# Kernel tuning notes

Measured on AMD Instinct MI355X. Metric: run time of the kernel, lower is better.

## Reference

```python
import jax, jax.numpy as jnp
import numpy as np

B, N, F_IN, F_OUT, T, K = 2, 4096, 16, 16, 12, 3


def setup_inputs() -> dict:
    key = jax.random.key(0)
    k1, k2, k3, k4 = jax.random.split(key, 4)
    x = jax.random.normal(k1, (B, N, F_IN, T), dtype=jnp.float32)
    # stacked K Chebyshev polynomial matrices T_k(L~), each (N, N)
    cheb_polynomials = jax.random.normal(k2, (K, N, N), dtype=jnp.float32) / np.sqrt(N)
    # ChebNetII interpolation table: cheb_poly_xj[j, k] = T_k evaluated at node x_j (scalar)
    cheb_poly_xj = jax.random.normal(k3, (K, K), dtype=jnp.float32)
    # learned Gamma_j parameters, each (F_in, F_out)
    Gamma = jax.random.normal(k4, (K, F_IN, F_OUT), dtype=jnp.float32) * 0.1
    return {"x": x, "cheb_polynomials": cheb_polynomials,
            "cheb_poly_xj": cheb_poly_xj, "Gamma": Gamma}


def reference(x, cheb_polynomials, cheb_poly_xj, Gamma):
    # x: (B, N, F_in, T); cheb_polynomials: (K, N, N);
    # cheb_poly_xj: (K, K) scalars; Gamma: (K, F_in, F_out)
    K_ = Gamma.shape[0]
    # lhs_k = sum_j Gamma_j * cheb_poly_xj[j, k]  -> (K, F_in, F_out); hoisted out of T loop
    lhs = jnp.einsum('jio,jk->kio', Gamma, cheb_poly_xj)
    # project features first (small contraction): (K, B, N, F_out, T)
    z = jnp.einsum('bmft,kfo->kbmot', x, lhs)
    # graph propagation: rhs[b,n,f] = sum_m x[b,m,f] * T_k[m, n]  (note T_k applied on the right)
    out = jnp.einsum('kmn,kbmot->bnot', cheb_polynomials, z)
    return jax.nn.relu((2.0 / (K_ + 1)) * out)
```

## Files before the change

kernel.cpp:

```cpp
#include <hip/hip_runtime.h>
#include <stdint.h>

typedef float    f32x4 __attribute__((ext_vector_type(4)));
typedef _Float16 f16x8 __attribute__((ext_vector_type(8)));
typedef unsigned int u32x4 __attribute__((ext_vector_type(4)));

#define NN     4096
#define KTOT   12288
#define CDIM   384
#define BN     128
#define BK     32
#define TSTEPS 384

__global__ __launch_bounds__(256) void zbuild_kernel(
    const float* __restrict__ x,
    const float* __restrict__ xj,
    const float* __restrict__ gamma,
    _Float16* __restrict__ zws)
{
  __shared__ float xs[32 * 193];
  __shared__ float lhs[768];
  const int tid = threadIdx.x;
  const int b   = blockIdx.x & 1;
  const int m0  = (blockIdx.x >> 1) << 5;

  for (int e = tid; e < 768; e += 256) {
    const int k = e >> 8, fo = e & 255;
    float s = 0.f;
#pragma unroll
    for (int j = 0; j < 3; ++j) s += gamma[j * 256 + fo] * xj[j * 3 + k];
    lhs[e] = s;
  }
  const float* xsrc = x + (size_t)(b * 4096 + m0) * 192;
  for (int q = tid; q < 1536; q += 256) {
    const int fl  = q << 2;
    const int ml  = fl / 192;
    const int off = fl - ml * 192;
    const f32x4 v = *(const f32x4*)(xsrc + fl);
#pragma unroll
    for (int r = 0; r < 4; ++r) xs[ml * 193 + off + r] = v[r];
  }
  __syncthreads();

  for (int slot = tid; slot < 512; slot += 256) {
    const int ml = slot & 31, o = slot >> 5;
    float acc[3][12];
#pragma unroll
    for (int k = 0; k < 3; ++k)
#pragma unroll
      for (int t = 0; t < 12; ++t) acc[k][t] = 0.f;

#pragma unroll
    for (int f = 0; f < 16; ++f) {
      float xv[12];
#pragma unroll
      for (int t = 0; t < 12; ++t) xv[t] = xs[ml * 193 + f * 12 + t];
#pragma unroll
      for (int k = 0; k < 3; ++k) {
        const float lf = lhs[k * 256 + f * 16 + o];
#pragma unroll
        for (int t = 0; t < 12; ++t) acc[k][t] += xv[t] * lf;
      }
    }
    const int mg = m0 + ml;
    const int cb = b * 192 + o * 12;
#pragma unroll
    for (int k = 0; k < 3; ++k)
#pragma unroll
      for (int t = 0; t < 12; ++t)
        zws[(size_t)(cb + t) * KTOT + k * 4096 + mg] = (_Float16)acc[k][t];
  }
}

__global__ __launch_bounds__(512, 2) void gemm_kernel(
    const float* __restrict__ cheb,
    const _Float16* __restrict__ zws,
    float* __restrict__ partials,
    int S, int spb)
{
  __shared__ unsigned short As[2][CDIM * BK];
  __shared__ unsigned short Bs[2][BN * BK];

  const int tid  = threadIdx.x;
  const int by   = blockIdx.x % S;
  const int bx   = blockIdx.x / S;
  const int lane = tid & 63, wid = tid >> 6;
  const int l15  = lane & 15, l4 = lane >> 4;
  const int wc   = wid >> 1, wn = wid & 1;
  const int nbase = bx * BN;
  const int step0 = by * spb;
  int nsteps = TSTEPS - step0;
  if (nsteps > spb) nsteps = spb;
  if (nsteps < 0) nsteps = 0;

  f32x4 acc[6][4];
#pragma unroll
  for (int mi = 0; mi < 6; ++mi)
#pragma unroll
    for (int ni = 0; ni < 4; ++ni) acc[mi][ni] = (f32x4)(0.f);

  const int ia0 = wid * 192 + lane;
  const int rrB = tid >> 5;
  const int n4B = (tid & 31) << 2;

  u32x4 areg[3];
  f32x4 breg[2];

  auto LOADA = [&](int t) {
    const size_t mb = (size_t)(step0 + t) * (BK * 2);
#pragma unroll
    for (int j = 0; j < 3; ++j) {
      const int i = ia0 + j * 64;
      const char* p = (const char*)zws + (size_t)(i >> 2) * (KTOT * 2) + mb + (i & 3) * 16;
      areg[j] = *(const u32x4*)p;
    }
  };
  auto LOADB = [&](int t) {
    const int m0g = (step0 + t) * BK;
#pragma unroll
    for (int s = 0; s < 2; ++s) {
      const int m = rrB * 2 + s;
      breg[s] = *(const f32x4*)(cheb + (size_t)(m0g + m) * NN + nbase + n4B);
    }
  };
  auto WRITEA = [&](int buf) {
#pragma unroll
    for (int j = 0; j < 3; ++j) {
      const int i   = ia0 + j * 64;
      const int c   = i >> 2;
      const int blk = i ^ ((c >> 1) & 3);
      *(u32x4*)&As[buf][blk * 8] = areg[j];
    }
  };
  auto WRITEB = [&](int buf) {
#pragma unroll
    for (int d = 0; d < 4; ++d) {
      const _Float16 h0 = (_Float16)breg[0][d];
      const _Float16 h1 = (_Float16)breg[1][d];
      const int n   = n4B + d;
      const int us0 = n * BK + rrB * 2;
      int blk = us0 >> 3;
      blk ^= (n >> 2) & 7;
      const int usp = blk * 8 + (us0 & 7);
      const uint32_t w = (uint32_t)__builtin_bit_cast(unsigned short, h0) |
                         ((uint32_t)__builtin_bit_cast(unsigned short, h1) << 16);
      *(uint32_t*)&Bs[buf][usp] = w;
    }
  };
  auto COMPUTE = [&](int cur) {
    f16x8 af[6];
#pragma unroll
    for (int mi = 0; mi < 6; ++mi) {
      const int c   = wc * 96 + mi * 16 + l15;
      const int i   = c * 4 + l4;
      const int blk = i ^ ((c >> 1) & 3);
      af[mi] = *(const f16x8*)&As[cur][blk * 8];
    }
    f16x8 bf[4];
#pragma unroll
    for (int ni = 0; ni < 4; ++ni) {
      const int n   = wn * 64 + ni * 16 + l15;
      const int blk = (n * 4 + l4) ^ ((n >> 2) & 7);
      bf[ni] = *(const f16x8*)&Bs[cur][blk * 8];
    }
#pragma unroll
    for (int mi = 0; mi < 6; ++mi)
#pragma unroll
      for (int ni = 0; ni < 4; ++ni)
        acc[mi][ni] = __builtin_amdgcn_mfma_f32_16x16x32_f16(
            af[mi], bf[ni], acc[mi][ni], 0, 0, 0);
  };

  if (nsteps > 0) {
    LOADA(0); LOADB(0);
    WRITEA(0); WRITEB(0);
    __syncthreads();
    for (int t = 0; t < nsteps; ++t) {
      const int cur = t & 1;
      const bool pf = (t + 1 < nsteps);
      if (pf) { LOADA(t + 1); LOADB(t + 1); }
      COMPUTE(cur);
      if (pf) { WRITEA(cur ^ 1); WRITEB(cur ^ 1); }
      __syncthreads();
    }
  }

  float* pb = partials + (size_t)by * ((size_t)CDIM * NN);
#pragma unroll
  for (int mi = 0; mi < 6; ++mi) {
    const int c0 = wc * 96 + mi * 16 + l4 * 4;
#pragma unroll
    for (int ni = 0; ni < 4; ++ni) {
      const int n = nbase + wn * 64 + ni * 16 + l15;
#pragma unroll
      for (int r = 0; r < 4; ++r)
        pb[(size_t)(c0 + r) * NN + n] = acc[mi][ni][r];
    }
  }
}

__global__ __launch_bounds__(256) void reduce_kernel(
    const float* __restrict__ partials, float* __restrict__ out, int S)
{
  __shared__ float T[192 * 33];
  const int tid = threadIdx.x;
  const int n0  = blockIdx.x * 32;
  const int cb  = blockIdx.y;

  for (int i = tid; i < 6144; i += 256) {
    const int c_l = i >> 5, n_l = i & 31;
    const float* p = partials + (size_t)(cb * 192 + c_l) * NN + n0 + n_l;
    float s = 0.f;
    for (int ss = 0; ss < S; ++ss) s += p[(size_t)ss * ((size_t)CDIM * NN)];
    T[c_l * 33 + n_l] = s;
  }
  __syncthreads();
  for (int j = tid; j < 6144; j += 256) {
    const int n_l = j / 192, ot = j - n_l * 192;
    const float v = 0.5f * T[ot * 33 + n_l];
    out[(size_t)(cb * 4096 + n0 + n_l) * 192 + ot] = v > 0.f ? v : 0.f;
  }
}

extern "C" void kernel_launch(void* const* d_in, const int* in_sizes, int n_in,
                              void* d_out, int out_size, void* d_ws, size_t ws_size,
                              hipStream_t stream) {
  (void)in_sizes; (void)n_in; (void)out_size;
  const float* x     = (const float*)d_in[0];
  const float* cheb  = (const float*)d_in[1];
  const float* xj    = (const float*)d_in[2];
  const float* gamma = (const float*)d_in[3];
  float* out = (float*)d_out;

  const long long zbytes = (long long)CDIM * KTOT * 2;
  const long long pslab  = (long long)CDIM * NN * 4;
  int S = 8;
  const long long avail = (long long)ws_size - zbytes;
  if (avail < 8 * pslab) {
    S = (int)(avail / pslab);
    if (S < 1) S = 1;
    if (S > 8) S = 8;
  }
  const int spb = (TSTEPS + S - 1) / S;

  _Float16* zws   = (_Float16*)d_ws;
  float* partials = (float*)((char*)d_ws + zbytes);

  zbuild_kernel<<<256, 256, 0, stream>>>(x, xj, gamma, zws);
  gemm_kernel<<<32 * S, 512, 0, stream>>>(cheb, zws, partials, S, spb);
  reduce_kernel<<<dim3(128, 2), 256, 0, stream>>>(partials, out, S);
}
```

Baseline: 365.5 us.

## Load GEMM A fragments directly to registers, halve N tile, raise occupancy

The GEMM no longer stages the z operand (A) in shared memory. Each wave loads its MFMA A fragments straight from global memory into registers, double-buffered across steps. The N tile drops from 128 to 64, doubling the block count, and launch bounds now allow 4 blocks per CU since shared memory only holds B. This removes LDS traffic and bank conflicts for A, at the cost of more global/L2 reads of A (each block re-reads it for a smaller N slice) and less B reuse per block.

```diff
diff --git a/kernel.cpp b/kernel.cpp
--- a/kernel.cpp
+++ b/kernel.cpp
@@ -1,6 +1,7 @@
 #include <hip/hip_runtime.h>
 #include <stdint.h>
 
+typedef float    f32x2 __attribute__((ext_vector_type(2)));
 typedef float    f32x4 __attribute__((ext_vector_type(4)));
 typedef _Float16 f16x8 __attribute__((ext_vector_type(8)));
 typedef unsigned int u32x4 __attribute__((ext_vector_type(4)));
@@ -8,7 +9,7 @@
 #define NN     4096
 #define KTOT   12288
 #define CDIM   384
-#define BN     128
+#define BN     64
 #define BK     32
 #define TSTEPS 384
 
@@ -72,126 +73,102 @@
   }
 }
 
-__global__ __launch_bounds__(512, 2) void gemm_kernel(
+__global__ __launch_bounds__(512, 4) void gemm_kernel(
     const float* __restrict__ cheb,
     const _Float16* __restrict__ zws,
     float* __restrict__ partials,
     int S, int spb)
 {
-  __shared__ unsigned short As[2][CDIM * BK];
-  __shared__ unsigned short Bs[2][BN * BK];
+  __shared__ unsigned int Bs[2][BN * BK / 2];
 
   const int tid  = threadIdx.x;
   const int by   = blockIdx.x % S;
   const int bx   = blockIdx.x / S;
   const int lane = tid & 63, wid = tid >> 6;
   const int l15  = lane & 15, l4 = lane >> 4;
-  const int wc   = wid >> 1, wn = wid & 1;
   const int nbase = bx * BN;
   const int step0 = by * spb;
   int nsteps = TSTEPS - step0;
   if (nsteps > spb) nsteps = spb;
   if (nsteps < 0) nsteps = 0;
 
-  f32x4 acc[6][4];
-#pragma unroll
-  for (int mi = 0; mi < 6; ++mi)
+  f32x4 acc[3][4];
+#pragma unroll
+  for (int mi = 0; mi < 3; ++mi)
 #pragma unroll
     for (int ni = 0; ni < 4; ++ni) acc[mi][ni] = (f32x4)(0.f);
 
-  const int ia0 = wid * 192 + lane;
-  const int rrB = tid >> 5;
-  const int n4B = (tid & 31) << 2;
-
-  u32x4 areg[3];
-  f32x4 breg[2];
-
-  auto LOADA = [&](int t) {
-    const size_t mb = (size_t)(step0 + t) * (BK * 2);
-#pragma unroll
-    for (int j = 0; j < 3; ++j) {
-      const int i = ia0 + j * 64;
-      const char* p = (const char*)zws + (size_t)(i >> 2) * (KTOT * 2) + mb + (i & 3) * 16;
-      areg[j] = *(const u32x4*)p;
-    }
-  };
+  const int rr = tid >> 5;
+  const int nn = (tid & 31) << 1;
+  f32x2 b0, b1;
   auto LOADB = [&](int t) {
-    const int m0g = (step0 + t) * BK;
-#pragma unroll
-    for (int s = 0; s < 2; ++s) {
-      const int m = rrB * 2 + s;
-      breg[s] = *(const f32x4*)(cheb + (size_t)(m0g + m) * NN + nbase + n4B);
-    }
-  };
-  auto WRITEA = [&](int buf) {
-#pragma unroll
-    for (int j = 0; j < 3; ++j) {
-      const int i   = ia0 + j * 64;
-      const int c   = i >> 2;
-      const int blk = i ^ ((c >> 1) & 3);
-      *(u32x4*)&As[buf][blk * 8] = areg[j];
-    }
+    const float* base = cheb + (size_t)(step0 + t) * BK * NN + nbase + nn;
+    b0 = *(const f32x2*)(base + (size_t)(2 * rr)     * NN);
+    b1 = *(const f32x2*)(base + (size_t)(2 * rr + 1) * NN);
   };
   auto WRITEB = [&](int buf) {
 #pragma unroll
-    for (int d = 0; d < 4; ++d) {
-      const _Float16 h0 = (_Float16)breg[0][d];
-      const _Float16 h1 = (_Float16)breg[1][d];
-      const int n   = n4B + d;
-      const int us0 = n * BK + rrB * 2;
-      int blk = us0 >> 3;
-      blk ^= (n >> 2) & 7;
-      const int usp = blk * 8 + (us0 & 7);
+    for (int d = 0; d < 2; ++d) {
+      const int n = nn + d;
+      const _Float16 h0 = (_Float16)b0[d], h1 = (_Float16)b1[d];
       const uint32_t w = (uint32_t)__builtin_bit_cast(unsigned short, h0) |
                          ((uint32_t)__builtin_bit_cast(unsigned short, h1) << 16);
-      *(uint32_t*)&Bs[buf][usp] = w;
-    }
-  };
-  auto COMPUTE = [&](int cur) {
-    f16x8 af[6];
-#pragma unroll
-    for (int mi = 0; mi < 6; ++mi) {
-      const int c   = wc * 96 + mi * 16 + l15;
-      const int i   = c * 4 + l4;
-      const int blk = i ^ ((c >> 1) & 3);
-      af[mi] = *(const f16x8*)&As[cur][blk * 8];
-    }
+      const int blk = (n * 4 + (rr >> 2)) ^ ((n >> 2) & 3);
+      Bs[buf][blk * 4 + (rr & 3)] = w;
+    }
+  };
+
+  const char* abase = (const char*)zws +
+      (size_t)(wid * 48 + l15) * (KTOT * 2) + (size_t)l4 * 16;
+  auto LOADA = [&](int t, u32x4* ar) {
+    const size_t kb = (size_t)(step0 + t) * (BK * 2);
+#pragma unroll
+    for (int mi = 0; mi < 3; ++mi)
+      ar[mi] = *(const u32x4*)(abase + (size_t)mi * 16 * (KTOT * 2) + kb);
+  };
+
+  auto STEP = [&](int t, u32x4* arCur, u32x4* arNxt, int cur) {
+    const bool pf = (t + 1 < nsteps);
+    if (pf) LOADB(t + 1);
     f16x8 bf[4];
 #pragma unroll
     for (int ni = 0; ni < 4; ++ni) {
-      const int n   = wn * 64 + ni * 16 + l15;
-      const int blk = (n * 4 + l4) ^ ((n >> 2) & 7);
-      bf[ni] = *(const f16x8*)&Bs[cur][blk * 8];
-    }
-#pragma unroll
-    for (int mi = 0; mi < 6; ++mi)
+      const int n   = ni * 16 + l15;
+      const int blk = (n * 4 + l4) ^ ((n >> 2) & 3);
+      bf[ni] = *(const f16x8*)&Bs[cur][blk * 4];
+    }
+    if (pf) LOADA(t + 1, arNxt);
+#pragma unroll
+    for (int mi = 0; mi < 3; ++mi) {
+      const f16x8 af = __builtin_bit_cast(f16x8, arCur[mi]);
 #pragma unroll
       for (int ni = 0; ni < 4; ++ni)
         acc[mi][ni] = __builtin_amdgcn_mfma_f32_16x16x32_f16(
-            af[mi], bf[ni], acc[mi][ni], 0, 0, 0);
-  };
-
+            af, bf[ni], acc[mi][ni], 0, 0, 0);
+    }
+    if (pf) WRITEB(cur ^ 1);
+    __syncthreads();
+  };
+
+  u32x4 arA[3], arB[3];
   if (nsteps > 0) {
-    LOADA(0); LOADB(0);
-    WRITEA(0); WRITEB(0);
+    LOADB(0); WRITEB(0); LOADA(0, arA);
     __syncthreads();
-    for (int t = 0; t < nsteps; ++t) {
-      const int cur = t & 1;
-      const bool pf = (t + 1 < nsteps);
-      if (pf) { LOADA(t + 1); LOADB(t + 1); }
-      COMPUTE(cur);
-      if (pf) { WRITEA(cur ^ 1); WRITEB(cur ^ 1); }
-      __syncthreads();
-    }
+    int t = 0;
+    for (; t + 1 < nsteps; t += 2) {
+      STEP(t,     arA, arB, t & 1);
+      STEP(t + 1, arB, arA, (t + 1) & 1);
+    }
+    if (t < nsteps) STEP(t, arA, arB, t & 1);
   }
 
   float* pb = partials + (size_t)by * ((size_t)CDIM * NN);
 #pragma unroll
-  for (int mi = 0; mi < 6; ++mi) {
-    const int c0 = wc * 96 + mi * 16 + l4 * 4;
+  for (int mi = 0; mi < 3; ++mi) {
+    const int c0 = wid * 48 + mi * 16 + l4 * 4;
 #pragma unroll
     for (int ni = 0; ni < 4; ++ni) {
-      const int n = nbase + wn * 64 + ni * 16 + l15;
+      const int n = nbase + ni * 16 + l15;
 #pragma unroll
       for (int r = 0; r < 4; ++r)
         pb[(size_t)(c0 + r) * NN + n] = acc[mi][ni][r];
@@ -247,6 +224,6 @@
   float* partials = (float*)((char*)d_ws + zbytes);
 
   zbuild_kernel<<<256, 256, 0, stream>>>(x, xj, gamma, zws);
-  gemm_kernel<<<32 * S, 512, 0, stream>>>(cheb, zws, partials, S, spb);
+  gemm_kernel<<<(NN / BN) * S, 512, 0, stream>>>(cheb, zws, partials, S, spb);
   reduce_kernel<<<dim3(128, 2), 256, 0, stream>>>(partials, out, S);
 }
```

After: 413.8 us. 1.13x slower.
